# Kernel optimization log

Measured on AMD Instinct MI355X. Metric: run time of the kernel, lower is better.

The kernel has to match this reference:

```python
import jax, jax.numpy as jnp
import numpy as np

EPS = 1e-4  # matches torch: x.norm(2, dim=1, keepdim=True) + 0.0001

def setup_inputs() -> dict:
    key = jax.random.key(0)
    k1, k2, k3 = jax.random.split(key, 3)
    B, IN, OUT = 16384, 2048, 2048
    x = jax.random.normal(k1, (B, IN), dtype=jnp.float32)
    # nn.Linear default init: U(-1/sqrt(in), 1/sqrt(in))
    bound = 1.0 / np.sqrt(IN)
    W = jax.random.uniform(k2, (OUT, IN), dtype=jnp.float32, minval=-bound, maxval=bound)
    b = jax.random.uniform(k3, (OUT,), dtype=jnp.float32, minval=-bound, maxval=bound)
    return {"x": x, "W": W, "b": b}

def reference(x, W, b):
    # L2-normalize each row, then Linear, then ReLU
    norm = jnp.linalg.norm(x, ord=2, axis=1, keepdims=True)  # [B, 1]
    x_dir = x / (norm + EPS)
    h = jnp.einsum('bi,oi->bo', x_dir, W) + b  # [B, OUT]
    return jax.nn.relu(h)
```

## Files before the change

### kernel.cpp

```cpp
#include <hip/hip_runtime.h>
#include <hip/hip_bf16.h>
#include <stdint.h>

#define B_ROWS 16384
#define IN_DIM 2048
#define OUT_DIM 2048

typedef __attribute__((ext_vector_type(4))) float f32x4;
typedef __attribute__((ext_vector_type(8))) short s16x8;

__device__ __forceinline__ unsigned short f2bf_rne(float f) {
  union { float f; unsigned u; } c; c.f = f;
  unsigned u = c.u;
  return (unsigned short)((u + 0x7FFFu + ((u >> 16) & 1u)) >> 16);
}

#define PREP_X_BLOCKS 4096
#define PREP_W_BLOCKS 2048

__global__ void __launch_bounds__(256) prep_kernel(const float* __restrict__ x,
                                                   unsigned short* __restrict__ xn,
                                                   float* __restrict__ scale,
                                                   const float* __restrict__ W,
                                                   unsigned short* __restrict__ Wb) {
  if (blockIdx.x < PREP_X_BLOCKS) {
    const int row  = (blockIdx.x * 256 + threadIdx.x) >> 6;
    const int lane = threadIdx.x & 63;
    const float4* xr = (const float4*)(x + (size_t)row * IN_DIM);
    unsigned short* xrow = xn + (size_t)row * IN_DIM;

    float ss = 0.0f;
    #pragma unroll
    for (int j = 0; j < 4; ++j) {
      const int f4 = j * 128 + lane * 2;
      float4 v0 = xr[f4 + 0];
      float4 v1 = xr[f4 + 1];
      ss += v0.x * v0.x + v0.y * v0.y + v0.z * v0.z + v0.w * v0.w +
            v1.x * v1.x + v1.y * v1.y + v1.z * v1.z + v1.w * v1.w;
      s16x8 p;
      p[0] = (short)f2bf_rne(v0.x); p[1] = (short)f2bf_rne(v0.y);
      p[2] = (short)f2bf_rne(v0.z); p[3] = (short)f2bf_rne(v0.w);
      p[4] = (short)f2bf_rne(v1.x); p[5] = (short)f2bf_rne(v1.y);
      p[6] = (short)f2bf_rne(v1.z); p[7] = (short)f2bf_rne(v1.w);
      *(s16x8*)(xrow + f4 * 4) = p;
    }

    #pragma unroll
    for (int m = 32; m > 0; m >>= 1) ss += __shfl_xor(ss, m, 64);
    if (lane == 0) scale[row] = 1.0f / (sqrtf(ss) + 1e-4f);
  } else {
    const size_t base = (size_t)(blockIdx.x - PREP_X_BLOCKS) * 2048 +
                        (size_t)threadIdx.x * 8;
    const float4* wp = (const float4*)(W + base);
    float4 v0 = wp[0];
    float4 v1 = wp[1];
    s16x8 p;
    p[0] = (short)f2bf_rne(v0.x); p[1] = (short)f2bf_rne(v0.y);
    p[2] = (short)f2bf_rne(v0.z); p[3] = (short)f2bf_rne(v0.w);
    p[4] = (short)f2bf_rne(v1.x); p[5] = (short)f2bf_rne(v1.y);
    p[6] = (short)f2bf_rne(v1.z); p[7] = (short)f2bf_rne(v1.w);
    *(s16x8*)(Wb + base) = p;
  }
}


#define GLD16(SRC, DST)                                                        \
  __builtin_amdgcn_global_load_lds(                                            \
      (const __attribute__((address_space(1))) unsigned int*)(SRC),            \
      (__attribute__((address_space(3))) unsigned int*)(DST), 16, 0, 0)

__global__ void __launch_bounds__(512, 1) gemm_kernel(const unsigned short* __restrict__ A,
                                                      const unsigned short* __restrict__ Bm,
                                                      const float* __restrict__ scale,
                                                      const float* __restrict__ bias,
                                                      float* __restrict__ out) {
  __shared__ unsigned short As[2][256 * 64];
  __shared__ unsigned short Bs[2][256 * 64];

  const int tid = threadIdx.x;
  const int bid = blockIdx.x;
  const int xcd = bid & 7;
  const int loc = bid >> 3;
  const int bm  = xcd * 8 + (loc >> 3);
  const int bn  = loc & 7;

  const int lane = tid & 63;
  const int wave = tid >> 6;
  const int wm   = wave >> 2;
  const int wn   = wave & 3;
  const int lrow = lane & 15;
  const int lq   = lane >> 4;

  const int sr = tid >> 3;
  const int sc = tid & 7;
  const unsigned short* aG = A  + (size_t)(bm * 256 + sr) * IN_DIM + ((sc ^ (sr & 7)) * 8);
  const unsigned short* bG = Bm + (size_t)(bn * 256 + sr) * IN_DIM + ((sc ^ (sr & 7)) * 8);

  const int aRow = (wm * 128 + lrow) * 64;
  const int bRow = (wn * 64  + lrow) * 64;
  const int c0   = (lq ^ (lrow & 7)) * 8;

  f32x4 acc[8][4] = {};
  s16x8 af[4] = {};
  s16x8 bf[4][2] = {};

  {
    char* aD = (char*)&As[0][0] + tid * 16;
    char* bD = (char*)&Bs[0][0] + tid * 16;
    GLD16(bG,                         bD);
    GLD16(bG + (size_t) 64 * IN_DIM,  bD + 8192);
    GLD16(bG + (size_t)128 * IN_DIM,  bD + 16384);
    GLD16(bG + (size_t)192 * IN_DIM,  bD + 24576);
    GLD16(aG,                         aD);
    GLD16(aG + (size_t)128 * IN_DIM,  aD + 16384);
    GLD16(aG + (size_t) 64 * IN_DIM,  aD + 8192);
    GLD16(aG + (size_t)192 * IN_DIM,  aD + 24576);
  }
  asm volatile("s_waitcnt vmcnt(2)" ::: "memory");
  __builtin_amdgcn_s_barrier();

  for (int T = 0; T < IN_DIM / 64; ++T) {
    const int cur = T & 1, nxt = cur ^ 1;
    const size_t kN = (size_t)((T < IN_DIM / 64 - 1) ? (T + 1) * 64 : 0);
    char* aD = (char*)&As[nxt][0] + tid * 16;
    char* bD = (char*)&Bs[nxt][0] + tid * 16;
    const unsigned short* aS = aG + kN;
    const unsigned short* bS = bG + kN;

    __builtin_amdgcn_s_setprio(1);
    #pragma unroll
    for (int mi = 0; mi < 4; ++mi)
      #pragma unroll
      for (int ni = 0; ni < 4; ++ni)
        acc[4 + mi][ni] = __builtin_amdgcn_mfma_f32_16x16x32_bf16(af[mi], bf[ni][1], acc[4 + mi][ni], 0, 0, 0);
    __builtin_amdgcn_s_setprio(0);
    #pragma unroll
    for (int ni = 0; ni < 4; ++ni) {
      bf[ni][0] = *(const s16x8*)(&Bs[cur][bRow + ni * 1024 + c0]);
      bf[ni][1] = *(const s16x8*)(&Bs[cur][bRow + ni * 1024 + (c0 ^ 32)]);
    }
    #pragma unroll
    for (int mi = 0; mi < 4; ++mi)
      af[mi] = *(const s16x8*)(&As[cur][aRow + mi * 1024 + c0]);
    GLD16(bS,                        bD);
    GLD16(bS + (size_t)64 * IN_DIM,  bD + 8192);
    __builtin_amdgcn_s_barrier();

    __builtin_amdgcn_s_setprio(1);
    #pragma unroll
    for (int mi = 0; mi < 4; ++mi)
      #pragma unroll
      for (int ni = 0; ni < 4; ++ni)
        acc[mi][ni] = __builtin_amdgcn_mfma_f32_16x16x32_bf16(af[mi], bf[ni][0], acc[mi][ni], 0, 0, 0);
    __builtin_amdgcn_s_setprio(0);
    #pragma unroll
    for (int mi = 0; mi < 4; ++mi)
      af[mi] = *(const s16x8*)(&As[cur][aRow + mi * 1024 + (c0 ^ 32)]);
    GLD16(bS + (size_t)128 * IN_DIM, bD + 16384);
    GLD16(bS + (size_t)192 * IN_DIM, bD + 24576);
    asm volatile("s_waitcnt vmcnt(4)" ::: "memory");
    __builtin_amdgcn_s_barrier();

    __builtin_amdgcn_s_setprio(1);
    #pragma unroll
    for (int mi = 0; mi < 4; ++mi)
      #pragma unroll
      for (int ni = 0; ni < 4; ++ni)
        acc[mi][ni] = __builtin_amdgcn_mfma_f32_16x16x32_bf16(af[mi], bf[ni][1], acc[mi][ni], 0, 0, 0);
    __builtin_amdgcn_s_setprio(0);
    #pragma unroll
    for (int mi = 0; mi < 4; ++mi)
      af[mi] = *(const s16x8*)(&As[cur][aRow + (4 + mi) * 1024 + c0]);
    GLD16(aS,                        aD);
    GLD16(aS + (size_t)128 * IN_DIM, aD + 16384);
    __builtin_amdgcn_s_barrier();

    __builtin_amdgcn_s_setprio(1);
    #pragma unroll
    for (int mi = 0; mi < 4; ++mi)
      #pragma unroll
      for (int ni = 0; ni < 4; ++ni)
        acc[4 + mi][ni] = __builtin_amdgcn_mfma_f32_16x16x32_bf16(af[mi], bf[ni][0], acc[4 + mi][ni], 0, 0, 0);
    __builtin_amdgcn_s_setprio(0);
    #pragma unroll
    for (int mi = 0; mi < 4; ++mi)
      af[mi] = *(const s16x8*)(&As[cur][aRow + (4 + mi) * 1024 + (c0 ^ 32)]);
    GLD16(aS + (size_t)64  * IN_DIM, aD + 8192);
    GLD16(aS + (size_t)192 * IN_DIM, aD + 24576);
    asm volatile("s_waitcnt vmcnt(2)" ::: "memory");
    __builtin_amdgcn_s_barrier();
  }

  __builtin_amdgcn_s_setprio(1);
  #pragma unroll
  for (int mi = 0; mi < 4; ++mi)
    #pragma unroll
    for (int ni = 0; ni < 4; ++ni)
      acc[4 + mi][ni] = __builtin_amdgcn_mfma_f32_16x16x32_bf16(af[mi], bf[ni][1], acc[4 + mi][ni], 0, 0, 0);
  __builtin_amdgcn_s_setprio(0);

  const int row0 = bm * 256 + wm * 128 + lq * 4;
  const int col0 = bn * 256 + wn * 64 + lrow;
  #pragma unroll
  for (int mi = 0; mi < 8; ++mi) {
    const int row = row0 + mi * 16;
    const f32x4 sc4 = *(const f32x4*)(scale + row);
    #pragma unroll
    for (int ni = 0; ni < 4; ++ni) {
      const int col = col0 + ni * 16;
      const float bcol = bias[col];
      #pragma unroll
      for (int r = 0; r < 4; ++r) {
        float v = acc[mi][ni][r] * sc4[r] + bcol;
        out[(size_t)(row + r) * OUT_DIM + col] = fmaxf(v, 0.0f);
      }
    }
  }
}

extern "C" void kernel_launch(void* const* d_in, const int* in_sizes, int n_in,
                              void* d_out, int out_size, void* d_ws, size_t ws_size,
                              hipStream_t stream) {
  const float* x = (const float*)d_in[0];
  const float* W = (const float*)d_in[1];
  const float* b = (const float*)d_in[2];
  float* out = (float*)d_out;

  char* ws = (char*)d_ws;
  unsigned short* xn    = (unsigned short*)ws;
  unsigned short* Wb    = (unsigned short*)(ws + (size_t)67108864);
  float*          scale = (float*)(ws + (size_t)67108864 + (size_t)8388608);

  prep_kernel<<<PREP_X_BLOCKS + PREP_W_BLOCKS, 256, 0, stream>>>(x, xn, scale, W, Wb);

  gemm_kernel<<<(OUT_DIM / 256) * (B_ROWS / 256), 512, 0, stream>>>(xn, Wb, scale, b, out);
}
```

Measured before the change: 363.3 us.

## Replace software-pipelined fragment prefetch with load-then-compute phases per K-step

The GEMM main loop used to overlap MFMA work on previously loaded register fragments with LDS reads for the next phase, carrying af/bf across phases and finishing with an epilogue MFMA block. It is now restructured into four sequential phases. Each phase loads its A fragments (and B fragments where needed) from LDS, issues global-to-LDS prefetches, hits a barrier, runs its MFMAs, then hits a second barrier. This simplifies the register lifetimes and lowers pressure, but adds barriers per K-step and gives up the overlap of LDS reads with MFMA execution.

```diff
diff --git a/kernel.cpp b/kernel.cpp
--- a/kernel.cpp
+++ b/kernel.cpp
@@ -101,8 +101,7 @@
   const int c0   = (lq ^ (lrow & 7)) * 8;
 
   f32x4 acc[8][4] = {};
-  s16x8 af[4] = {};
-  s16x8 bf[4][2] = {};
+  s16x8 bf[4][2];
 
   {
     char* aD = (char*)&As[0][0] + tid * 16;
@@ -126,78 +125,89 @@
     char* bD = (char*)&Bs[nxt][0] + tid * 16;
     const unsigned short* aS = aG + kN;
     const unsigned short* bS = bG + kN;
-
-    __builtin_amdgcn_s_setprio(1);
-    #pragma unroll
-    for (int mi = 0; mi < 4; ++mi)
+    const unsigned short* Ac = &As[cur][0];
+    const unsigned short* Bc = &Bs[cur][0];
+
+    {
+      s16x8 a[4];
+      #pragma unroll
+      for (int mi = 0; mi < 4; ++mi)
+        a[mi] = *(const s16x8*)(Ac + aRow + mi * 1024 + c0);
       #pragma unroll
       for (int ni = 0; ni < 4; ++ni)
-        acc[4 + mi][ni] = __builtin_amdgcn_mfma_f32_16x16x32_bf16(af[mi], bf[ni][1], acc[4 + mi][ni], 0, 0, 0);
-    __builtin_amdgcn_s_setprio(0);
-    #pragma unroll
-    for (int ni = 0; ni < 4; ++ni) {
-      bf[ni][0] = *(const s16x8*)(&Bs[cur][bRow + ni * 1024 + c0]);
-      bf[ni][1] = *(const s16x8*)(&Bs[cur][bRow + ni * 1024 + (c0 ^ 32)]);
-    }
-    #pragma unroll
-    for (int mi = 0; mi < 4; ++mi)
-      af[mi] = *(const s16x8*)(&As[cur][aRow + mi * 1024 + c0]);
-    GLD16(bS,                        bD);
-    GLD16(bS + (size_t)64 * IN_DIM,  bD + 8192);
-    __builtin_amdgcn_s_barrier();
-
-    __builtin_amdgcn_s_setprio(1);
-    #pragma unroll
-    for (int mi = 0; mi < 4; ++mi)
+        bf[ni][0] = *(const s16x8*)(Bc + bRow + ni * 1024 + c0);
+      GLD16(bS,                        bD);
+      GLD16(bS + (size_t)64 * IN_DIM,  bD + 8192);
+      __builtin_amdgcn_s_barrier();
+      __builtin_amdgcn_s_setprio(1);
+      #pragma unroll
+      for (int mi = 0; mi < 4; ++mi)
+        #pragma unroll
+        for (int ni = 0; ni < 4; ++ni)
+          acc[mi][ni] = __builtin_amdgcn_mfma_f32_16x16x32_bf16(a[mi], bf[ni][0], acc[mi][ni], 0, 0, 0);
+      __builtin_amdgcn_s_setprio(0);
+      __builtin_amdgcn_s_barrier();
+    }
+
+    {
+      s16x8 a[4];
+      #pragma unroll
+      for (int mi = 0; mi < 4; ++mi)
+        a[mi] = *(const s16x8*)(Ac + aRow + mi * 1024 + (c0 ^ 32));
       #pragma unroll
       for (int ni = 0; ni < 4; ++ni)
-        acc[mi][ni] = __builtin_amdgcn_mfma_f32_16x16x32_bf16(af[mi], bf[ni][0], acc[mi][ni], 0, 0, 0);
-    __builtin_amdgcn_s_setprio(0);
-    #pragma unroll
-    for (int mi = 0; mi < 4; ++mi)
-      af[mi] = *(const s16x8*)(&As[cur][aRow + mi * 1024 + (c0 ^ 32)]);
-    GLD16(bS + (size_t)128 * IN_DIM, bD + 16384);
-    GLD16(bS + (size_t)192 * IN_DIM, bD + 24576);
-    asm volatile("s_waitcnt vmcnt(4)" ::: "memory");
-    __builtin_amdgcn_s_barrier();
-
-    __builtin_amdgcn_s_setprio(1);
-    #pragma unroll
-    for (int mi = 0; mi < 4; ++mi)
-      #pragma unroll
-      for (int ni = 0; ni < 4; ++ni)
-        acc[mi][ni] = __builtin_amdgcn_mfma_f32_16x16x32_bf16(af[mi], bf[ni][1], acc[mi][ni], 0, 0, 0);
-    __builtin_amdgcn_s_setprio(0);
-    #pragma unroll
-    for (int mi = 0; mi < 4; ++mi)
-      af[mi] = *(const s16x8*)(&As[cur][aRow + (4 + mi) * 1024 + c0]);
-    GLD16(aS,                        aD);
-    GLD16(aS + (size_t)128 * IN_DIM, aD + 16384);
-    __builtin_amdgcn_s_barrier();
-
-    __builtin_amdgcn_s_setprio(1);
-    #pragma unroll
-    for (int mi = 0; mi < 4; ++mi)
-      #pragma unroll
-      for (int ni = 0; ni < 4; ++ni)
-        acc[4 + mi][ni] = __builtin_amdgcn_mfma_f32_16x16x32_bf16(af[mi], bf[ni][0], acc[4 + mi][ni], 0, 0, 0);
-    __builtin_amdgcn_s_setprio(0);
-    #pragma unroll
-    for (int mi = 0; mi < 4; ++mi)
-      af[mi] = *(const s16x8*)(&As[cur][aRow + (4 + mi) * 1024 + (c0 ^ 32)]);
-    GLD16(aS + (size_t)64  * IN_DIM, aD + 8192);
-    GLD16(aS + (size_t)192 * IN_DIM, aD + 24576);
-    asm volatile("s_waitcnt vmcnt(2)" ::: "memory");
-    __builtin_amdgcn_s_barrier();
-  }
-
-  __builtin_amdgcn_s_setprio(1);
-  #pragma unroll
-  for (int mi = 0; mi < 4; ++mi)
-    #pragma unroll
-    for (int ni = 0; ni < 4; ++ni)
-      acc[4 + mi][ni] = __builtin_amdgcn_mfma_f32_16x16x32_bf16(af[mi], bf[ni][1], acc[4 + mi][ni], 0, 0, 0);
-  __builtin_amdgcn_s_setprio(0);
+        bf[ni][1] = *(const s16x8*)(Bc + bRow + ni * 1024 + (c0 ^ 32));
+      GLD16(bS + (size_t)128 * IN_DIM, bD + 16384);
+      GLD16(bS + (size_t)192 * IN_DIM, bD + 24576);
+      __builtin_amdgcn_s_barrier();
+      __builtin_amdgcn_s_setprio(1);
+      #pragma unroll
+      for (int mi = 0; mi < 4; ++mi)
+        #pragma unroll
+        for (int ni = 0; ni < 4; ++ni)
+          acc[mi][ni] = __builtin_amdgcn_mfma_f32_16x16x32_bf16(a[mi], bf[ni][1], acc[mi][ni], 0, 0, 0);
+      __builtin_amdgcn_s_setprio(0);
+      asm volatile("s_waitcnt vmcnt(4)" ::: "memory");
+      __builtin_amdgcn_s_barrier();
+    }
+
+    {
+      s16x8 a[4];
+      #pragma unroll
+      for (int mi = 0; mi < 4; ++mi)
+        a[mi] = *(const s16x8*)(Ac + aRow + (4 + mi) * 1024 + c0);
+      GLD16(aS,                        aD);
+      GLD16(aS + (size_t)128 * IN_DIM, aD + 16384);
+      __builtin_amdgcn_s_barrier();
+      __builtin_amdgcn_s_setprio(1);
+      #pragma unroll
+      for (int mi = 0; mi < 4; ++mi)
+        #pragma unroll
+        for (int ni = 0; ni < 4; ++ni)
+          acc[4 + mi][ni] = __builtin_amdgcn_mfma_f32_16x16x32_bf16(a[mi], bf[ni][0], acc[4 + mi][ni], 0, 0, 0);
+      __builtin_amdgcn_s_setprio(0);
+      __builtin_amdgcn_s_barrier();
+    }
+
+    {
+      s16x8 a[4];
+      #pragma unroll
+      for (int mi = 0; mi < 4; ++mi)
+        a[mi] = *(const s16x8*)(Ac + aRow + (4 + mi) * 1024 + (c0 ^ 32));
+      GLD16(aS + (size_t)64  * IN_DIM, aD + 8192);
+      GLD16(aS + (size_t)192 * IN_DIM, aD + 24576);
+      __builtin_amdgcn_s_barrier();
+      __builtin_amdgcn_s_setprio(1);
+      #pragma unroll
+      for (int mi = 0; mi < 4; ++mi)
+        #pragma unroll
+        for (int ni = 0; ni < 4; ++ni)
+          acc[4 + mi][ni] = __builtin_amdgcn_mfma_f32_16x16x32_bf16(a[mi], bf[ni][1], acc[4 + mi][ni], 0, 0, 0);
+      __builtin_amdgcn_s_setprio(0);
+      asm volatile("s_waitcnt vmcnt(2)" ::: "memory");
+      __builtin_amdgcn_s_barrier();
+    }
+  }
 
   const int row0 = bm * 256 + wm * 128 + lq * 4;
   const int col0 = bn * 256 + wn * 64 + lrow;
```

After: 356.4 us. No clear change (-1.9%).

## Restructure GEMM main loop into software-pipelined 4-phase schedule with two barriers

Applied to the files above, without the earlier changes.

Reorganizes the bf16 MFMA main loop so each K-tile runs in four compute phases with only two barriers instead of four. The A fragments are double-buffered in registers (aP/aQ), and the B half-tile for tile T+2 is prefetched into the current LDS buffer early, so global loads and LDS reads overlap more with MFMA work. The aim is to cut barrier stalls and LDS-read latency exposure. In exchange it raises register pressure and adds more delicate hazards between LDS writes and reads.

```diff
diff --git a/kernel.cpp b/kernel.cpp
--- a/kernel.cpp
+++ b/kernel.cpp
@@ -101,12 +101,13 @@
   const int c0   = (lq ^ (lrow & 7)) * 8;
 
   f32x4 acc[8][4] = {};
-  s16x8 af[4] = {};
-  s16x8 bf[4][2] = {};
+  s16x8 aP[4], aQ[4];
+  s16x8 bf[4][2];
 
   {
     char* aD = (char*)&As[0][0] + tid * 16;
     char* bD = (char*)&Bs[0][0] + tid * 16;
+    char* bD1 = (char*)&Bs[1][0] + tid * 16;
     GLD16(bG,                         bD);
     GLD16(bG + (size_t) 64 * IN_DIM,  bD + 8192);
     GLD16(bG + (size_t)128 * IN_DIM,  bD + 16384);
@@ -115,89 +116,93 @@
     GLD16(aG + (size_t)128 * IN_DIM,  aD + 16384);
     GLD16(aG + (size_t) 64 * IN_DIM,  aD + 8192);
     GLD16(aG + (size_t)192 * IN_DIM,  aD + 24576);
-  }
-  asm volatile("s_waitcnt vmcnt(2)" ::: "memory");
+    GLD16(bG + 64,                        bD1);
+    GLD16(bG + 64 + (size_t)64 * IN_DIM,  bD1 + 8192);
+  }
+  asm volatile("s_waitcnt vmcnt(4)" ::: "memory");
   __builtin_amdgcn_s_barrier();
+
+  #pragma unroll
+  for (int mi = 0; mi < 4; ++mi)
+    aP[mi] = *(const s16x8*)(&As[0][aRow + mi * 1024 + c0]);
+  #pragma unroll
+  for (int ni = 0; ni < 4; ++ni)
+    bf[ni][0] = *(const s16x8*)(&Bs[0][bRow + ni * 1024 + c0]);
 
   for (int T = 0; T < IN_DIM / 64; ++T) {
     const int cur = T & 1, nxt = cur ^ 1;
-    const size_t kN = (size_t)((T < IN_DIM / 64 - 1) ? (T + 1) * 64 : 0);
-    char* aD = (char*)&As[nxt][0] + tid * 16;
-    char* bD = (char*)&Bs[nxt][0] + tid * 16;
-    const unsigned short* aS = aG + kN;
-    const unsigned short* bS = bG + kN;
-
-    __builtin_amdgcn_s_setprio(1);
-    #pragma unroll
-    for (int mi = 0; mi < 4; ++mi)
-      #pragma unroll
-      for (int ni = 0; ni < 4; ++ni)
-        acc[4 + mi][ni] = __builtin_amdgcn_mfma_f32_16x16x32_bf16(af[mi], bf[ni][1], acc[4 + mi][ni], 0, 0, 0);
-    __builtin_amdgcn_s_setprio(0);
-    #pragma unroll
-    for (int ni = 0; ni < 4; ++ni) {
-      bf[ni][0] = *(const s16x8*)(&Bs[cur][bRow + ni * 1024 + c0]);
-      bf[ni][1] = *(const s16x8*)(&Bs[cur][bRow + ni * 1024 + (c0 ^ 32)]);
-    }
-    #pragma unroll
-    for (int mi = 0; mi < 4; ++mi)
-      af[mi] = *(const s16x8*)(&As[cur][aRow + mi * 1024 + c0]);
-    GLD16(bS,                        bD);
-    GLD16(bS + (size_t)64 * IN_DIM,  bD + 8192);
-    __builtin_amdgcn_s_barrier();
-
-    __builtin_amdgcn_s_setprio(1);
-    #pragma unroll
-    for (int mi = 0; mi < 4; ++mi)
-      #pragma unroll
-      for (int ni = 0; ni < 4; ++ni)
-        acc[mi][ni] = __builtin_amdgcn_mfma_f32_16x16x32_bf16(af[mi], bf[ni][0], acc[mi][ni], 0, 0, 0);
-    __builtin_amdgcn_s_setprio(0);
-    #pragma unroll
-    for (int mi = 0; mi < 4; ++mi)
-      af[mi] = *(const s16x8*)(&As[cur][aRow + mi * 1024 + (c0 ^ 32)]);
-    GLD16(bS + (size_t)128 * IN_DIM, bD + 16384);
-    GLD16(bS + (size_t)192 * IN_DIM, bD + 24576);
+    const unsigned short* Ac = &As[cur][0];
+    const unsigned short* Bc = &Bs[cur][0];
+    const unsigned short* An = &As[nxt][0];
+    const unsigned short* Bn = &Bs[nxt][0];
+    char* aD  = (char*)&As[nxt][0] + tid * 16;
+    char* bD  = (char*)&Bs[nxt][0] + tid * 16;
+    char* bDc = (char*)&Bs[cur][0] + tid * 16;
+    const size_t k1 = (size_t)((T < 31) ? (T + 1) * 64 : 0);
+    const size_t k2 = (size_t)((T < 30) ? (T + 2) * 64 : 0);
+
+    #pragma unroll
+    for (int mi = 0; mi < 4; ++mi)
+      aQ[mi] = *(const s16x8*)(Ac + aRow + mi * 1024 + (c0 ^ 32));
+    #pragma unroll
+    for (int ni = 0; ni < 4; ++ni)
+      bf[ni][1] = *(const s16x8*)(Bc + bRow + ni * 1024 + (c0 ^ 32));
+    GLD16(aG + k1,                         aD);
+    GLD16(aG + k1 + (size_t)128 * IN_DIM,  aD + 16384);
+    __builtin_amdgcn_s_setprio(1);
+    #pragma unroll
+    for (int mi = 0; mi < 4; ++mi)
+      #pragma unroll
+      for (int ni = 0; ni < 4; ++ni)
+        acc[mi][ni] = __builtin_amdgcn_mfma_f32_16x16x32_bf16(aP[mi], bf[ni][0], acc[mi][ni], 0, 0, 0);
+    __builtin_amdgcn_s_setprio(0);
     asm volatile("s_waitcnt vmcnt(4)" ::: "memory");
     __builtin_amdgcn_s_barrier();
 
-    __builtin_amdgcn_s_setprio(1);
-    #pragma unroll
-    for (int mi = 0; mi < 4; ++mi)
-      #pragma unroll
-      for (int ni = 0; ni < 4; ++ni)
-        acc[mi][ni] = __builtin_amdgcn_mfma_f32_16x16x32_bf16(af[mi], bf[ni][1], acc[mi][ni], 0, 0, 0);
-    __builtin_amdgcn_s_setprio(0);
-    #pragma unroll
-    for (int mi = 0; mi < 4; ++mi)
-      af[mi] = *(const s16x8*)(&As[cur][aRow + (4 + mi) * 1024 + c0]);
-    GLD16(aS,                        aD);
-    GLD16(aS + (size_t)128 * IN_DIM, aD + 16384);
-    __builtin_amdgcn_s_barrier();
-
-    __builtin_amdgcn_s_setprio(1);
-    #pragma unroll
-    for (int mi = 0; mi < 4; ++mi)
-      #pragma unroll
-      for (int ni = 0; ni < 4; ++ni)
-        acc[4 + mi][ni] = __builtin_amdgcn_mfma_f32_16x16x32_bf16(af[mi], bf[ni][0], acc[4 + mi][ni], 0, 0, 0);
-    __builtin_amdgcn_s_setprio(0);
-    #pragma unroll
-    for (int mi = 0; mi < 4; ++mi)
-      af[mi] = *(const s16x8*)(&As[cur][aRow + (4 + mi) * 1024 + (c0 ^ 32)]);
-    GLD16(aS + (size_t)64  * IN_DIM, aD + 8192);
-    GLD16(aS + (size_t)192 * IN_DIM, aD + 24576);
+    #pragma unroll
+    for (int mi = 0; mi < 4; ++mi)
+      aP[mi] = *(const s16x8*)(Ac + aRow + (4 + mi) * 1024 + c0);
+    GLD16(bG + k1 + (size_t)128 * IN_DIM,  bD + 16384);
+    GLD16(bG + k1 + (size_t)192 * IN_DIM,  bD + 24576);
+    __builtin_amdgcn_s_setprio(1);
+    #pragma unroll
+    for (int mi = 0; mi < 4; ++mi)
+      #pragma unroll
+      for (int ni = 0; ni < 4; ++ni)
+        acc[mi][ni] = __builtin_amdgcn_mfma_f32_16x16x32_bf16(aQ[mi], bf[ni][1], acc[mi][ni], 0, 0, 0);
+    __builtin_amdgcn_s_setprio(0);
+
+    #pragma unroll
+    for (int mi = 0; mi < 4; ++mi)
+      aQ[mi] = *(const s16x8*)(Ac + aRow + (4 + mi) * 1024 + (c0 ^ 32));
+    GLD16(aG + k1 + (size_t) 64 * IN_DIM,  aD + 8192);
+    GLD16(aG + k1 + (size_t)192 * IN_DIM,  aD + 24576);
+    __builtin_amdgcn_s_setprio(1);
+    #pragma unroll
+    for (int mi = 0; mi < 4; ++mi)
+      #pragma unroll
+      for (int ni = 0; ni < 4; ++ni)
+        acc[4 + mi][ni] = __builtin_amdgcn_mfma_f32_16x16x32_bf16(aP[mi], bf[ni][0], acc[4 + mi][ni], 0, 0, 0);
+    __builtin_amdgcn_s_setprio(0);
     asm volatile("s_waitcnt vmcnt(2)" ::: "memory");
     __builtin_amdgcn_s_barrier();
-  }
-
-  __builtin_amdgcn_s_setprio(1);
-  #pragma unroll
-  for (int mi = 0; mi < 4; ++mi)
+
+    #pragma unroll
+    for (int mi = 0; mi < 4; ++mi)
+      aP[mi] = *(const s16x8*)(An + aRow + mi * 1024 + c0);
     #pragma unroll
     for (int ni = 0; ni < 4; ++ni)
-      acc[4 + mi][ni] = __builtin_amdgcn_mfma_f32_16x16x32_bf16(af[mi], bf[ni][1], acc[4 + mi][ni], 0, 0, 0);
-  __builtin_amdgcn_s_setprio(0);
+      bf[ni][0] = *(const s16x8*)(Bn + bRow + ni * 1024 + c0);
+    GLD16(bG + k2,                         bDc);
+    GLD16(bG + k2 + (size_t) 64 * IN_DIM,  bDc + 8192);
+    __builtin_amdgcn_s_setprio(1);
+    #pragma unroll
+    for (int mi = 0; mi < 4; ++mi)
+      #pragma unroll
+      for (int ni = 0; ni < 4; ++ni)
+        acc[4 + mi][ni] = __builtin_amdgcn_mfma_f32_16x16x32_bf16(aQ[mi], bf[ni][1], acc[4 + mi][ni], 0, 0, 0);
+    __builtin_amdgcn_s_setprio(0);
+  }
 
   const int row0 = bm * 256 + wm * 128 + lq * 4;
   const int col0 = bn * 256 + wn * 64 + lrow;
```

Result: no change. 365.6 us (+0.6%).
